# Kernel tuning notes

Measured on AMD Instinct MI355X. Metric: run time of the kernel, lower is better.

Reference implementation:

```python
import jax, jax.numpy as jnp
import numpy as np

# ---- Cl(3,0) algebra tables (basis: 1, e1, e2, e3, e12, e13, e23, e123) ----
def _build_algebra():
    dim = 8
    blades = sorted(range(dim), key=lambda b: (bin(b).count('1'), b))
    idx = {b: i for i, b in enumerate(blades)}
    C = np.zeros((dim, dim, dim), np.float32)
    for a in range(dim):
        for b in range(dim):
            s = 0; ash = a >> 1
            while ash:
                s += bin(ash & b).count('1'); ash >>= 1
            C[idx[a], idx[b], idx[a ^ b]] = -1.0 if (s & 1) else 1.0
    grades = np.array([bin(b).count('1') for b in blades])
    rev = np.array([(-1.0) ** (g * (g - 1) // 2) for g in grades], np.float32)
    gmask = np.zeros((4, dim), np.float32)
    gmask[grades, np.arange(dim)] = 1.0
    return C, rev, gmask, grades

_C_np, _REV_np, _GM_np, _GRADES = _build_algebra()
CAYLEY = jnp.asarray(_C_np)          # [8,8,8] sparse multiplication table
REV = jnp.asarray(_REV_np)           # reverse signs per blade
GMASK = jnp.asarray(_GM_np)          # [4,8] grade selector
BV_IDX = jnp.asarray(np.where(_GRADES == 2)[0])  # bivector slots [4,5,6]
G1_IDX = jnp.asarray(np.where(_GRADES == 1)[0])  # vector slots [1,2,3]

EPS = 1e-6
H_NUM, DEPTH, A_NUM, DISC, TEMP = 8, 3, 5, 0.99, 1.0

def gp(a, b):
    return jnp.einsum('...i,...j,ijk->...k', a, b, CAYLEY)

def reverse(x):
    return x * REV

def grade_energy(x):  # [...,8] -> [...,4] per-grade sum of squares
    return jnp.einsum('...d,gd->...g', x * x, GMASK)

def scatter_bv(c):  # [...,3] bivector coeffs -> full multivector [...,8]
    out = jnp.zeros(c.shape[:-1] + (8,), c.dtype)
    return out.at[..., BV_IDX].set(c)

def mv_exp_biv(b):  # exp of pure bivector in Cl(3,0): cos|B| + sinc|B| * B
    t = jnp.sqrt(jnp.sum(b * b, -1))
    small = t < 1e-6
    ts = jnp.where(small, 1.0, t)
    sinc = jnp.where(small, 1.0 - t * t / 6.0, jnp.sin(ts) / ts)
    return (sinc[..., None] * b).at[..., 0].add(jnp.cos(t))

def clayernorm(x, w):  # normalize by mean multivector norm across channels
    n = jnp.sqrt(jnp.sum(x * x, -1) + EPS)          # [...,C]
    denom = jnp.mean(n, -1, keepdims=True)[..., None] + EPS
    return x * w[:, None] / denom

def ggelu(x):  # gate multivector by GELU of its norm
    n = jnp.sqrt(jnp.sum(x * x, -1, keepdims=True) + EPS)
    return x * jax.nn.gelu(n) / (n + EPS)

def clinear(x, W, b):  # channel-mixing per blade: [O,C]x[...,C,8]
    return jnp.einsum('oc,...cd->...od', W, x) + b

def rotor_apply(x, bv):  # per-channel rotor sandwich, bv [C,3]
    R = mv_exp_biv(-0.5 * scatter_bv(bv))  # [C,8]
    return gp(gp(R, x), reverse(R))

def predict(x, nw, lw, lb, vw, vb, pw, pb):
    h = clayernorm(x, nw)
    h = clinear(h, lw, lb)
    h = ggelu(h)
    value = h[..., 0] @ vw + vb                      # grade-0 -> [N,1]
    g1 = h[..., G1_IDX].reshape(h.shape[0], -1)       # grade-1 flat
    policy = g1 @ pw + pb                             # [N,A]
    return policy, value

def dynamics(x, action, act_bv, nw, rbv, lw, lb, rw, rb):
    bv = act_bv[action]                               # [N,3]
    R = mv_exp_biv(-0.5 * scatter_bv(bv))[:, None, :]  # [N,1,8]
    ns = gp(gp(R, x), reverse(R))                     # rotor sandwich
    h = clayernorm(ns, nw)
    h = ggelu(h)
    h = rotor_apply(h, rbv)
    h = clinear(h, lw, lb)
    ns = ns + h                                       # residual GA block
    reward = ns[..., 0] @ rw + rb
    return reward, ns


def setup_inputs() -> dict:
    key = jax.random.key(0)
    ks = jax.random.split(key, 16)
    B, C, mid = 512, 256, 128
    f = jnp.float32
    return {
        'state': jax.random.normal(ks[0], (B, C, 8), f),
        'hyp_bv': jax.random.normal(ks[1], (H_NUM, 3), f) * 0.05,
        'sp_w1': jax.random.normal(ks[2], (4, 32), f) * 0.3,
        'sp_b1': jnp.zeros((32,), f),
        'sp_w2': jax.random.normal(ks[3], (32, 1), f) * 0.3,
        'sp_b2': jnp.zeros((1,), f),
        'p_norm_w': jnp.ones((C,), f),
        'p_lin_w': jax.random.normal(ks[4], (mid, C), f) / np.sqrt(C),
        'p_lin_b': jnp.zeros((mid, 8), f),
        'p_vw': jax.random.normal(ks[5], (mid, 1), f) * 0.1,
        'p_vb': jnp.zeros((1,), f),
        'p_pw': jax.random.normal(ks[6], (mid * 3, A_NUM), f) * 0.1,
        'p_pb': jnp.zeros((A_NUM,), f),
        'act_bv': jax.random.normal(ks[7], (A_NUM, 3), f) * 0.1,
        'd_norm_w': jnp.ones((C,), f),
        'd_rotor_bv': jax.random.normal(ks[8], (C, 3), f) * 0.05,
        'd_lin_w': jax.random.normal(ks[9], (C, C), f) / np.sqrt(C),
        'd_lin_b': jnp.zeros((C, 8), f),
        'd_rw': jax.random.normal(ks[10], (C, 1), f) * 0.1,
        'd_rb': jnp.zeros((1,), f),
    }


def reference(state, hyp_bv, sp_w1, sp_b1, sp_w2, sp_b2,
              p_norm_w, p_lin_w, p_lin_b, p_vw, p_vb, p_pw, p_pb,
              act_bv, d_norm_w, d_rotor_bv, d_lin_w, d_lin_b, d_rw, d_rb):
    B, C, D = state.shape
    H, A = H_NUM, A_NUM
    # hypothesis generation: H independent rotors applied to state
    R = mv_exp_biv(-0.5 * scatter_bv(hyp_bv))          # [H,8]
    hyp = gp(gp(R[None, :, None, :], state[:, None, :, :]),
             reverse(R)[None, :, None, :])             # [B,H,C,8]
    # exploration parameter from grade-norm features
    norms = jnp.sqrt(grade_energy(state) + 1e-12)       # [B,C,4]
    pooled = norms.mean(1)                              # [B,4]
    theta = jnp.maximum(pooled @ sp_w1 + sp_b1, 0.0) @ sp_w2 + sp_b2
    explore = jnp.abs(jnp.tanh(theta))                  # [B,1]
    N = B * H
    hf = hyp.reshape(N, C, D)
    exp_bh = jnp.broadcast_to(explore[:, None, :], (B, H, 1)).reshape(N, 1)
    noise = jax.random.normal(jax.random.key(42), (DEPTH, N, A), state.dtype) * 0.3
    hyp_values = jnp.zeros((B, H), state.dtype)
    first_actions = jnp.zeros((N,), jnp.int32)
    for d in range(DEPTH):  # fixed small depth loop; H vectorized
        policy, value = predict(hf, p_norm_w, p_lin_w, p_lin_b, p_vw, p_vb, p_pw, p_pb)
        bv_e = grade_energy(hf)[:, :, 2].mean(1, keepdims=True)  # bivector energy
        scores = policy + exp_bh * bv_e * noise[d]
        action = jnp.argmax(scores, -1)
        if d == 0:
            first_actions = action
        reward, hf = dynamics(hf, action, act_bv, d_norm_w, d_rotor_bv,
                              d_lin_w, d_lin_b, d_rw, d_rb)
        hyp_values = hyp_values + (DISC ** d) * reward.reshape(B, H)
    _, tv = predict(hf, p_norm_w, p_lin_w, p_lin_b, p_vw, p_vb, p_pw, p_pb)
    hyp_values = hyp_values + (DISC ** DEPTH) * tv.reshape(B, H)
    weights = jax.nn.softmax(hyp_values / TEMP, -1)     # [B,H]
    oh = jax.nn.one_hot(first_actions.reshape(B, H), A, dtype=state.dtype)
    ap = jnp.sum(weights[..., None] * oh, 1)            # [B,A]
    return ap / jnp.clip(jnp.sum(ap, -1, keepdims=True), 1e-8)
```

## Files before the change

### kernel.cpp

```cpp
#include <hip/hip_runtime.h>
#include <math.h>


#define NOISE_MODE 0
#define DEV static __device__ __forceinline__

constexpr int Bz = 512;
constexpr int Cz = 256;
constexpr int MIDz = 128;
constexpr int Hz = 8;
constexpr int Nz = 4096;
constexpr int Az = 5;
constexpr int NOISE_PER_D = Nz * Az;

constexpr size_t OFF_ROTH  = 0;
constexpr size_t OFF_ROTA  = OFF_ROTH + 64;
constexpr size_t OFF_ROTC  = OFF_ROTA + 40;
constexpr size_t OFF_EXPL  = OFF_ROTC + 2048;
constexpr size_t OFF_HV    = OFF_EXPL + 512;
constexpr size_t OFF_FIRST = OFF_HV + 4096;
constexpr size_t OFF_WTP   = OFF_FIRST + 4096;
constexpr size_t OFF_WTD   = OFF_WTP + (size_t)Cz * MIDz;
constexpr size_t OFF_A     = OFF_WTD + (size_t)Cz * Cz;

DEV void gp8(const float* a, const float* b, float* c) {
  c[0] = a[0]*b[0]+a[1]*b[1]+a[2]*b[2]+a[3]*b[3]-a[4]*b[4]-a[5]*b[5]-a[6]*b[6]-a[7]*b[7];
  c[1] = a[0]*b[1]+a[1]*b[0]-a[2]*b[4]-a[3]*b[5]+a[4]*b[2]+a[5]*b[3]-a[6]*b[7]-a[7]*b[6];
  c[2] = a[0]*b[2]+a[2]*b[0]+a[1]*b[4]-a[4]*b[1]-a[3]*b[6]+a[6]*b[3]+a[5]*b[7]+a[7]*b[5];
  c[3] = a[0]*b[3]+a[3]*b[0]+a[1]*b[5]-a[5]*b[1]+a[2]*b[6]-a[6]*b[2]-a[4]*b[7]-a[7]*b[4];
  c[4] = a[0]*b[4]+a[4]*b[0]+a[1]*b[2]-a[2]*b[1]-a[5]*b[6]+a[6]*b[5]+a[3]*b[7]+a[7]*b[3];
  c[5] = a[0]*b[5]+a[5]*b[0]+a[1]*b[3]-a[3]*b[1]+a[4]*b[6]-a[6]*b[4]-a[2]*b[7]-a[7]*b[2];
  c[6] = a[0]*b[6]+a[6]*b[0]+a[2]*b[3]-a[3]*b[2]-a[4]*b[5]+a[5]*b[4]+a[1]*b[7]+a[7]*b[1];
  c[7] = a[0]*b[7]+a[7]*b[0]+a[1]*b[6]+a[6]*b[1]+a[3]*b[4]+a[4]*b[3]-a[2]*b[5]-a[5]*b[2];
}

DEV void sandwich8(const float* R, const float* x, float* y) {
  float t[8];
  gp8(R, x, t);
  float Rr[8] = {R[0], R[1], R[2], R[3], -R[4], -R[5], -R[6], -R[7]};
  gp8(t, Rr, y);
}

DEV void rotor_from_bv(const float* bv, float* R) {
  float c4 = -0.5f * bv[0], c5 = -0.5f * bv[1], c6 = -0.5f * bv[2];
  float t = sqrtf(c4*c4 + c5*c5 + c6*c6);
  float sinc = (t < 1e-6f) ? (1.0f - t*t/6.0f) : (sinf(t)/t);
  R[0] = cosf(t); R[1] = 0.f; R[2] = 0.f; R[3] = 0.f;
  R[4] = sinc*c4; R[5] = sinc*c5; R[6] = sinc*c6; R[7] = 0.f;
}

DEV unsigned tf_rotl(unsigned v, int n) { return (v << n) | (v >> (32 - n)); }

DEV void threefry2x32(unsigned x0, unsigned x1, unsigned& o0, unsigned& o1) {
  const unsigned k0 = 0u, k1 = 42u;
  const unsigned k2 = k0 ^ k1 ^ 0x1BD11BDAu;
  x0 += k0; x1 += k1;
#define TF_R(r) { x0 += x1; x1 = tf_rotl(x1, r); x1 ^= x0; }
  TF_R(13) TF_R(15) TF_R(26) TF_R(6)
  x0 += k1; x1 += k2 + 1u;
  TF_R(17) TF_R(29) TF_R(16) TF_R(24)
  x0 += k2; x1 += k0 + 2u;
  TF_R(13) TF_R(15) TF_R(26) TF_R(6)
  x0 += k0; x1 += k1 + 3u;
  TF_R(17) TF_R(29) TF_R(16) TF_R(24)
  x0 += k1; x1 += k2 + 4u;
  TF_R(13) TF_R(15) TF_R(26) TF_R(6)
  x0 += k2; x1 += k0 + 5u;
#undef TF_R
  o0 = x0; o1 = x1;
}

DEV float erfinv32(float x) {
  float w = -log1pf(-x * x);
  float p;
  if (w < 5.0f) {
    w = w - 2.5f;
    p = 2.81022636e-08f;
    p = fmaf(p, w, 3.43273939e-07f);
    p = fmaf(p, w, -3.5233877e-06f);
    p = fmaf(p, w, -4.39150654e-06f);
    p = fmaf(p, w, 0.00021858087f);
    p = fmaf(p, w, -0.00125372503f);
    p = fmaf(p, w, -0.00417768164f);
    p = fmaf(p, w, 0.246640727f);
    p = fmaf(p, w, 1.50140941f);
  } else {
    w = sqrtf(w) - 3.0f;
    p = -0.000200214257f;
    p = fmaf(p, w, 0.000100950558f);
    p = fmaf(p, w, 0.00134934322f);
    p = fmaf(p, w, -0.00367342844f);
    p = fmaf(p, w, 0.00573950773f);
    p = fmaf(p, w, -0.0076224613f);
    p = fmaf(p, w, 0.00943887047f);
    p = fmaf(p, w, 1.00167406f);
    p = fmaf(p, w, 2.83297682f);
  }
  return p * x;
}

DEV float noise_val(int d, int r, int a) {
  unsigned idx = (unsigned)(d * NOISE_PER_D + r * Az + a);
  unsigned o0, o1, bits;
#if NOISE_MODE == 0
  threefry2x32(0u, idx, o0, o1);
  bits = o0 ^ o1;
#elif NOISE_MODE == 1
  const unsigned HALF = (unsigned)(3 * NOISE_PER_D) / 2u;
  unsigned j = (idx < HALF) ? idx : idx - HALF;
  threefry2x32(j, j + HALF, o0, o1);
  bits = (idx < HALF) ? o0 : o1;
#elif NOISE_MODE == 2
  threefry2x32(0u, idx, o0, o1);
  bits = o1;
#else
  threefry2x32(0u, idx, o0, o1);
  bits = o0;
#endif
  const float MINV = __uint_as_float(0xBF7FFFFFu);
  float f = __uint_as_float((bits >> 9) | 0x3F800000u) - 1.0f;
  float u = fmaxf(MINV, f * 2.0f + MINV);
  const float SQRT2 = __uint_as_float(0x3FB504F3u);
  return (SQRT2 * erfinv32(u)) * 0.3f;
}

DEV float gelu_tanh(float x) {
  float x3 = (x * x) * x;
  float t = tanhf(0.7978845608028654f * (x + 0.044715f * x3));
  return x * (0.5f * (1.0f + t));
}

DEV void pred_gemm(const float4* __restrict__ X, int l, float invd,
                   const float* __restrict__ WtP, const float* __restrict__ plb,
                   float hh[2][8]) {
  float pacc[2][8] = {{0,0,0,0,0,0,0,0},{0,0,0,0,0,0,0,0}};
  const float2* Wp2 = (const float2*)WtP;
#pragma unroll 4
  for (int c = 0; c < Cz; c++) {
    float4 xa = X[c], xb = X[Cz + c];
    float xv[8] = {xa.x, xa.y, xa.z, xa.w, xb.x, xb.y, xb.z, xb.w};
    float2 wv = Wp2[(size_t)c * 64 + l];
#pragma unroll
    for (int dd = 0; dd < 8; dd++) {
      pacc[0][dd] = fmaf(wv.x, xv[dd], pacc[0][dd]);
      pacc[1][dd] = fmaf(wv.y, xv[dd], pacc[1][dd]);
    }
  }
#pragma unroll
  for (int j = 0; j < 2; j++) {
    int o = 2 * l + j;
    float nsq = 0.f;
#pragma unroll
    for (int dd = 0; dd < 8; dd++) {
      hh[j][dd] = fmaf(pacc[j][dd], invd, plb[o * 8 + dd]);
      nsq += hh[j][dd] * hh[j][dd];
    }
    float nn = sqrtf(nsq + 1e-6f);
    float sc = gelu_tanh(nn) / (nn + 1e-6f);
#pragma unroll
    for (int dd = 0; dd < 8; dd++) hh[j][dd] *= sc;
  }
}


__global__ void k_prep(const float* __restrict__ hyp_bv, const float* __restrict__ act_bv,
                       const float* __restrict__ rot_bv, const float* __restrict__ plw,
                       const float* __restrict__ pnw, const float* __restrict__ dlw,
                       float* __restrict__ rotH, float* __restrict__ rotA,
                       float* __restrict__ rotC, float* __restrict__ hyp_val,
                       float* __restrict__ WtP, float* __restrict__ WtD) {
  int t = blockIdx.x * 256 + threadIdx.x;
  if (t < Cz * Cz)   { int c = t >> 8, o = t & 255; WtD[t] = dlw[o * Cz + c]; }
  if (t < Cz * MIDz) { int c = t >> 7, o = t & 127; WtP[t] = plw[o * Cz + c] * pnw[c]; }
  if (t < Nz) hyp_val[t] = 0.f;
  if (t < 8) rotor_from_bv(hyp_bv + t * 3, rotH + t * 8);
  else if (t < 13) rotor_from_bv(act_bv + (t - 8) * 3, rotA + (t - 8) * 8);
  else if (t >= 16 && t < 16 + Cz) rotor_from_bv(rot_bv + (t - 16) * 3, rotC + (t - 16) * 8);
}

__global__ void k_explore(const float* __restrict__ state, const float* __restrict__ w1,
                          const float* __restrict__ b1, const float* __restrict__ w2,
                          const float* __restrict__ b2, float* __restrict__ explore) {
  int b = blockIdx.x, c = threadIdx.x;
  const float4* xp = (const float4*)(state + ((size_t)b * Cz + c) * 8);
  float4 lo = xp[0], hi = xp[1];
  float g0 = lo.x * lo.x;
  float g1 = lo.y * lo.y + lo.z * lo.z + lo.w * lo.w;
  float g2 = hi.x * hi.x + hi.y * hi.y + hi.z * hi.z;
  float g3 = hi.w * hi.w;
  __shared__ float4 sm[256];
  sm[c] = make_float4(sqrtf(g0 + 1e-12f), sqrtf(g1 + 1e-12f),
                      sqrtf(g2 + 1e-12f), sqrtf(g3 + 1e-12f));
  __syncthreads();
  for (int s = 128; s > 0; s >>= 1) {
    if (c < s) {
      sm[c].x += sm[c + s].x; sm[c].y += sm[c + s].y;
      sm[c].z += sm[c + s].z; sm[c].w += sm[c + s].w;
    }
    __syncthreads();
  }
  if (c == 0) {
    float pooled[4] = {sm[0].x / 256.f, sm[0].y / 256.f, sm[0].z / 256.f, sm[0].w / 256.f};
    float theta = b2[0];
    for (int j = 0; j < 32; j++) {
      float hj = b1[j];
      for (int g = 0; g < 4; g++) hj = fmaf(pooled[g], w1[g * 32 + j], hj);
      hj = fmaxf(hj, 0.f);
      theta = fmaf(hj, w2[j], theta);
    }
    explore[b] = fabsf(tanhf(theta));
  }
}

__global__ __launch_bounds__(256, 4) void k_step(
    const float* __restrict__ src, float* __restrict__ dst, int apply_hyp,
    int dstep, int do_term,
    const float* __restrict__ rotH, const float* __restrict__ rotA,
    const float* __restrict__ rotC, const float* __restrict__ WtP,
    const float* __restrict__ plb, const float* __restrict__ pw,
    const float* __restrict__ pb, const float* __restrict__ vw,
    const float* __restrict__ vb, const float* __restrict__ dnw,
    const float* __restrict__ WtD, const float* __restrict__ dlb,
    const float* __restrict__ rw, const float* __restrict__ rb,
    const float* __restrict__ explore, float* __restrict__ hyp_val,
    int* __restrict__ first_act, float discf, float termdisc) {
  __shared__ float4 xs[4][2 * Cz];
  int w = threadIdx.x >> 6, l = threadIdx.x & 63;
  int r = blockIdx.x * 4 + w;
  int b = r >> 3, h = r & 7;
  float4* X = xs[w];
  const float* row = apply_hyp ? (src + (size_t)b * Cz * 8) : (src + (size_t)r * Cz * 8);
  float Rh[8];
  if (apply_hyp) {
#pragma unroll
    for (int i = 0; i < 8; i++) Rh[i] = rotH[h * 8 + i];
  }
  float nsum = 0.f, bsum = 0.f;
#pragma unroll
  for (int k = 0; k < 4; k++) {
    int c = 4 * l + k;
    const float4* xp = (const float4*)(row + (size_t)c * 8);
    float4 v0 = xp[0], v1 = xp[1];
    float x[8] = {v0.x, v0.y, v0.z, v0.w, v1.x, v1.y, v1.z, v1.w};
    if (apply_hyp) {
      float t[8];
      sandwich8(Rh, x, t);
#pragma unroll
      for (int i = 0; i < 8; i++) x[i] = t[i];
    }
    float ss = 0.f;
#pragma unroll
    for (int i = 0; i < 8; i++) ss += x[i] * x[i];
    nsum += sqrtf(ss + 1e-6f);
    bsum += x[4] * x[4] + x[5] * x[5] + x[6] * x[6];
    X[c]      = make_float4(x[0], x[1], x[2], x[3]);
    X[Cz + c] = make_float4(x[4], x[5], x[6], x[7]);
  }
#pragma unroll
  for (int m = 1; m < 64; m <<= 1) {
    nsum += __shfl_xor(nsum, m);
    bsum += __shfl_xor(bsum, m);
  }
  float invd = 1.0f / (nsum / 256.f + 1e-6f);
  float bv_e = bsum / 256.f;
  __syncthreads();

  float hh[2][8];
  pred_gemm(X, l, invd, WtP, plb, hh);
  float pol[Az] = {0, 0, 0, 0, 0};
#pragma unroll
  for (int j = 0; j < 2; j++) {
    int o = 2 * l + j;
#pragma unroll
    for (int k = 0; k < 3; k++) {
      float v = hh[j][1 + k];
      const float* pwj = pw + (size_t)(o * 3 + k) * Az;
#pragma unroll
      for (int a = 0; a < Az; a++) pol[a] = fmaf(v, pwj[a], pol[a]);
    }
  }
#pragma unroll
  for (int m = 1; m < 64; m <<= 1) {
#pragma unroll
    for (int a = 0; a < Az; a++) pol[a] += __shfl_xor(pol[a], m);
  }
  float coef = explore[b] * bv_e;
  float sa = -INFINITY;
  if (l < Az) sa = (pol[l] + pb[l]) + coef * noise_val(dstep, r, l);
  int best = 0;
  float bs = -INFINITY;
#pragma unroll
  for (int a = 0; a < Az; a++) {
    float s = __shfl(sa, a);
    if (s > bs) { bs = s; best = a; }
  }
  if (dstep == 0 && l == 0) first_act[r] = best;

  float Ra[8];
#pragma unroll
  for (int i = 0; i < 8; i++) Ra[i] = rotA[best * 8 + i];
  float y[4][8];
  float nsum2 = 0.f;
#pragma unroll
  for (int k = 0; k < 4; k++) {
    int c = 4 * l + k;
    float4 xa = X[c], xb = X[Cz + c];
    float x[8] = {xa.x, xa.y, xa.z, xa.w, xb.x, xb.y, xb.z, xb.w};
    sandwich8(Ra, x, y[k]);
    float ss = 0.f;
#pragma unroll
    for (int i = 0; i < 8; i++) ss += y[k][i] * y[k][i];
    nsum2 += sqrtf(ss + 1e-6f);
  }
#pragma unroll
  for (int m = 1; m < 64; m <<= 1) nsum2 += __shfl_xor(nsum2, m);
  float invd2 = 1.0f / (nsum2 / 256.f + 1e-6f);

#pragma unroll
  for (int k = 0; k < 4; k++) {
    int c = 4 * l + k;
    float sc = dnw[c] * invd2;
    float hch[8];
    float nsq = 0.f;
#pragma unroll
    for (int i = 0; i < 8; i++) { hch[i] = y[k][i] * sc; nsq += hch[i] * hch[i]; }
    float nn = sqrtf(nsq + 1e-6f);
    float ge = gelu_tanh(nn) / (nn + 1e-6f);
#pragma unroll
    for (int i = 0; i < 8; i++) hch[i] *= ge;
    float Rc[8];
    const float4* rp = (const float4*)(rotC + (size_t)c * 8);
    float4 r0 = rp[0], r1 = rp[1];
    Rc[0] = r0.x; Rc[1] = r0.y; Rc[2] = r0.z; Rc[3] = r0.w;
    Rc[4] = r1.x; Rc[5] = r1.y; Rc[6] = r1.z; Rc[7] = r1.w;
    float hp[8];
    sandwich8(Rc, hch, hp);
    X[c]      = make_float4(hp[0], hp[1], hp[2], hp[3]);
    X[Cz + c] = make_float4(hp[4], hp[5], hp[6], hp[7]);
  }
  __syncthreads();

  float acc[4][8];
#pragma unroll
  for (int g = 0; g < 4; g++) {
    int o = 4 * l + g;
#pragma unroll
    for (int dd = 0; dd < 8; dd++) acc[g][dd] = y[g][dd] + dlb[o * 8 + dd];
  }
  const float4* Wd4 = (const float4*)WtD;
#pragma unroll 4
  for (int c = 0; c < Cz; c++) {
    float4 xa = X[c], xb = X[Cz + c];
    float xv[8] = {xa.x, xa.y, xa.z, xa.w, xb.x, xb.y, xb.z, xb.w};
    float4 w4 = Wd4[(size_t)c * 64 + l];
#pragma unroll
    for (int dd = 0; dd < 8; dd++) {
      acc[0][dd] = fmaf(w4.x, xv[dd], acc[0][dd]);
      acc[1][dd] = fmaf(w4.y, xv[dd], acc[1][dd]);
      acc[2][dd] = fmaf(w4.z, xv[dd], acc[2][dd]);
      acc[3][dd] = fmaf(w4.w, xv[dd], acc[3][dd]);
    }
  }

  float rsum = 0.f;
  float hv_add;
  if (!do_term) {
    float* drow = dst + (size_t)r * Cz * 8;
#pragma unroll
    for (int g = 0; g < 4; g++) {
      int o = 4 * l + g;
      rsum = fmaf(acc[g][0], rw[o], rsum);
      float4* op = (float4*)(drow + (size_t)o * 8);
      op[0] = make_float4(acc[g][0], acc[g][1], acc[g][2], acc[g][3]);
      op[1] = make_float4(acc[g][4], acc[g][5], acc[g][6], acc[g][7]);
    }
#pragma unroll
    for (int m = 1; m < 64; m <<= 1) rsum += __shfl_xor(rsum, m);
    hv_add = discf * (rsum + rb[0]);
  } else {
    __syncthreads();
    float tsum = 0.f;
#pragma unroll
    for (int g = 0; g < 4; g++) {
      int o = 4 * l + g;
      rsum = fmaf(acc[g][0], rw[o], rsum);
      float ss = 0.f;
#pragma unroll
      for (int dd = 0; dd < 8; dd++) ss += acc[g][dd] * acc[g][dd];
      tsum += sqrtf(ss + 1e-6f);
      X[o]      = make_float4(acc[g][0], acc[g][1], acc[g][2], acc[g][3]);
      X[Cz + o] = make_float4(acc[g][4], acc[g][5], acc[g][6], acc[g][7]);
    }
#pragma unroll
    for (int m = 1; m < 64; m <<= 1) {
      rsum += __shfl_xor(rsum, m);
      tsum += __shfl_xor(tsum, m);
    }
    float invd3 = 1.0f / (tsum / 256.f + 1e-6f);
    __syncthreads();
    float th[2][8];
    pred_gemm(X, l, invd3, WtP, plb, th);
    float v = fmaf(th[0][0], vw[2 * l], th[1][0] * vw[2 * l + 1]);
#pragma unroll
    for (int m = 1; m < 64; m <<= 1) v += __shfl_xor(v, m);
    hv_add = discf * (rsum + rb[0]) + termdisc * (v + vb[0]);
  }
  if (l == 0) hyp_val[r] += hv_add;
}

__global__ void k_out(const float* __restrict__ hyp_val, const int* __restrict__ first_act,
                      float* __restrict__ out) {
  int b = blockIdx.x * blockDim.x + threadIdx.x;
  if (b >= Bz) return;
  float hv[Hz];
  float m = -INFINITY;
#pragma unroll
  for (int h = 0; h < Hz; h++) { hv[h] = hyp_val[b * Hz + h]; m = fmaxf(m, hv[h]); }
  float e[Hz];
  float se = 0.f;
#pragma unroll
  for (int h = 0; h < Hz; h++) { e[h] = expf(hv[h] - m); se += e[h]; }
  float ap[Az] = {0, 0, 0, 0, 0};
#pragma unroll
  for (int h = 0; h < Hz; h++) ap[first_act[b * Hz + h]] += e[h] / se;
  float tot = 0.f;
#pragma unroll
  for (int a = 0; a < Az; a++) tot += ap[a];
  float dn = fmaxf(tot, 1e-8f);
#pragma unroll
  for (int a = 0; a < Az; a++) out[b * Az + a] = ap[a] / dn;
}


extern "C" void kernel_launch(void* const* d_in, const int* in_sizes, int n_in,
                              void* d_out, int out_size, void* d_ws, size_t ws_size,
                              hipStream_t stream) {
  const float* state      = (const float*)d_in[0];
  const float* hyp_bv     = (const float*)d_in[1];
  const float* sp_w1      = (const float*)d_in[2];
  const float* sp_b1      = (const float*)d_in[3];
  const float* sp_w2      = (const float*)d_in[4];
  const float* sp_b2      = (const float*)d_in[5];
  const float* p_norm_w   = (const float*)d_in[6];
  const float* p_lin_w    = (const float*)d_in[7];
  const float* p_lin_b    = (const float*)d_in[8];
  const float* p_vw       = (const float*)d_in[9];
  const float* p_vb       = (const float*)d_in[10];
  const float* p_pw       = (const float*)d_in[11];
  const float* p_pb       = (const float*)d_in[12];
  const float* act_bv     = (const float*)d_in[13];
  const float* d_norm_w   = (const float*)d_in[14];
  const float* d_rotor_bv = (const float*)d_in[15];
  const float* d_lin_w    = (const float*)d_in[16];
  const float* d_lin_b    = (const float*)d_in[17];
  const float* d_rw       = (const float*)d_in[18];
  const float* d_rb       = (const float*)d_in[19];
  float* out = (float*)d_out;
  float* ws  = (float*)d_ws;

  float* rotH    = ws + OFF_ROTH;
  float* rotA    = ws + OFF_ROTA;
  float* rotC    = ws + OFF_ROTC;
  float* explore = ws + OFF_EXPL;
  float* hyp_val = ws + OFF_HV;
  int*   first   = (int*)(ws + OFF_FIRST);
  float* WtP     = ws + OFF_WTP;
  float* WtD     = ws + OFF_WTD;
  float* bufA    = ws + OFF_A;

  k_prep<<<256, 256, 0, stream>>>(hyp_bv, act_bv, d_rotor_bv, p_lin_w, p_norm_w,
                                  d_lin_w, rotH, rotA, rotC, hyp_val, WtP, WtD);
  k_explore<<<Bz, 256, 0, stream>>>(state, sp_w1, sp_b1, sp_w2, sp_b2, explore);

  const float d1 = 0.99f, d2 = 0.99f * 0.99f, d3 = 0.99f * 0.99f * 0.99f;
  k_step<<<Nz / 4, 256, 0, stream>>>(state, bufA, 1, 0, 0, rotH, rotA, rotC, WtP,
                                     p_lin_b, p_pw, p_pb, p_vw, p_vb, d_norm_w, WtD,
                                     d_lin_b, d_rw, d_rb, explore, hyp_val, first,
                                     1.0f, 0.f);
  k_step<<<Nz / 4, 256, 0, stream>>>(bufA, bufA, 0, 1, 0, rotH, rotA, rotC, WtP,
                                     p_lin_b, p_pw, p_pb, p_vw, p_vb, d_norm_w, WtD,
                                     d_lin_b, d_rw, d_rb, explore, hyp_val, first,
                                     d1, 0.f);
  k_step<<<Nz / 4, 256, 0, stream>>>(bufA, bufA, 0, 2, 1, rotH, rotA, rotC, WtP,
                                     p_lin_b, p_pw, p_pb, p_vw, p_vb, d_norm_w, WtD,
                                     d_lin_b, d_rw, d_rb, explore, hyp_val, first,
                                     d2, d3);
  k_out<<<2, 256, 0, stream>>>(hyp_val, first, out);
}
```

Before: 379.1 us.

## Use packed FP32 FMA and swizzle shared-memory channel layout in GEMMs

```diff
diff --git a/kernel.cpp b/kernel.cpp
--- a/kernel.cpp
+++ b/kernel.cpp
@@ -4,6 +4,9 @@
 
 #define NOISE_MODE 0
 #define DEV static __device__ __forceinline__
+
+typedef float v2f __attribute__((ext_vector_type(2)));
+DEV v2f fma2(v2f a, v2f b, v2f c) { return __builtin_elementwise_fma(a, b, c); }
 
 constexpr int Bz = 512;
 constexpr int Cz = 256;
@@ -130,20 +133,32 @@
   return x * (0.5f * (1.0f + t));
 }
 
+DEV int SL(int c) { return ((c & 3) << 6) + (c >> 2); }
+
 DEV void pred_gemm(const float4* __restrict__ X, int l, float invd,
                    const float* __restrict__ WtP, const float* __restrict__ plb,
                    float hh[2][8]) {
-  float pacc[2][8] = {{0,0,0,0,0,0,0,0},{0,0,0,0,0,0,0,0}};
+  v2f pacc[2][4] = {{{0,0},{0,0},{0,0},{0,0}},{{0,0},{0,0},{0,0},{0,0}}};
   const float2* Wp2 = (const float2*)WtP;
-#pragma unroll 4
-  for (int c = 0; c < Cz; c++) {
-    float4 xa = X[c], xb = X[Cz + c];
-    float xv[8] = {xa.x, xa.y, xa.z, xa.w, xb.x, xb.y, xb.z, xb.w};
-    float2 wv = Wp2[(size_t)c * 64 + l];
-#pragma unroll
-    for (int dd = 0; dd < 8; dd++) {
-      pacc[0][dd] = fmaf(wv.x, xv[dd], pacc[0][dd]);
-      pacc[1][dd] = fmaf(wv.y, xv[dd], pacc[1][dd]);
+#pragma unroll 2
+  for (int c4 = 0; c4 < 64; c4++) {
+#pragma unroll
+    for (int k = 0; k < 4; k++) {
+      int c = 4 * c4 + k;
+      float4 xa = X[(k << 6) + c4];
+      float4 xb = X[Cz + (k << 6) + c4];
+      float2 wv = Wp2[(size_t)c * 64 + l];
+      v2f w0 = {wv.x, wv.x}, w1 = {wv.y, wv.y};
+      v2f x0 = {xa.x, xa.y}, x1 = {xa.z, xa.w};
+      v2f x2 = {xb.x, xb.y}, x3 = {xb.z, xb.w};
+      pacc[0][0] = fma2(w0, x0, pacc[0][0]);
+      pacc[0][1] = fma2(w0, x1, pacc[0][1]);
+      pacc[0][2] = fma2(w0, x2, pacc[0][2]);
+      pacc[0][3] = fma2(w0, x3, pacc[0][3]);
+      pacc[1][0] = fma2(w1, x0, pacc[1][0]);
+      pacc[1][1] = fma2(w1, x1, pacc[1][1]);
+      pacc[1][2] = fma2(w1, x2, pacc[1][2]);
+      pacc[1][3] = fma2(w1, x3, pacc[1][3]);
     }
   }
 #pragma unroll
@@ -152,7 +167,8 @@
     float nsq = 0.f;
 #pragma unroll
     for (int dd = 0; dd < 8; dd++) {
-      hh[j][dd] = fmaf(pacc[j][dd], invd, plb[o * 8 + dd]);
+      float av = (dd & 1) ? pacc[j][dd >> 1].y : pacc[j][dd >> 1].x;
+      hh[j][dd] = fmaf(av, invd, plb[o * 8 + dd]);
       nsq += hh[j][dd] * hh[j][dd];
     }
     float nn = sqrtf(nsq + 1e-6f);
@@ -253,8 +269,9 @@
     for (int i = 0; i < 8; i++) ss += x[i] * x[i];
     nsum += sqrtf(ss + 1e-6f);
     bsum += x[4] * x[4] + x[5] * x[5] + x[6] * x[6];
-    X[c]      = make_float4(x[0], x[1], x[2], x[3]);
-    X[Cz + c] = make_float4(x[4], x[5], x[6], x[7]);
+    int sl = (k << 6) + l;
+    X[sl]      = make_float4(x[0], x[1], x[2], x[3]);
+    X[Cz + sl] = make_float4(x[4], x[5], x[6], x[7]);
   }
 #pragma unroll
   for (int m = 1; m < 64; m <<= 1) {
@@ -303,8 +320,8 @@
   float nsum2 = 0.f;
 #pragma unroll
   for (int k = 0; k < 4; k++) {
-    int c = 4 * l + k;
-    float4 xa = X[c], xb = X[Cz + c];
+    int sl = (k << 6) + l;
+    float4 xa = X[sl], xb = X[Cz + sl];
     float x[8] = {xa.x, xa.y, xa.z, xa.w, xb.x, xb.y, xb.z, xb.w};
     sandwich8(Ra, x, y[k]);
     float ss = 0.f;
@@ -335,30 +352,50 @@
     Rc[4] = r1.x; Rc[5] = r1.y; Rc[6] = r1.z; Rc[7] = r1.w;
     float hp[8];
     sandwich8(Rc, hch, hp);
-    X[c]      = make_float4(hp[0], hp[1], hp[2], hp[3]);
-    X[Cz + c] = make_float4(hp[4], hp[5], hp[6], hp[7]);
+    int sl = (k << 6) + l;
+    X[sl]      = make_float4(hp[0], hp[1], hp[2], hp[3]);
+    X[Cz + sl] = make_float4(hp[4], hp[5], hp[6], hp[7]);
   }
   __syncthreads();
 
-  float acc[4][8];
+  v2f acc[4][4];
 #pragma unroll
   for (int g = 0; g < 4; g++) {
     int o = 4 * l + g;
 #pragma unroll
-    for (int dd = 0; dd < 8; dd++) acc[g][dd] = y[g][dd] + dlb[o * 8 + dd];
+    for (int p = 0; p < 4; p++) {
+      acc[g][p].x = y[g][2 * p]     + dlb[o * 8 + 2 * p];
+      acc[g][p].y = y[g][2 * p + 1] + dlb[o * 8 + 2 * p + 1];
+    }
   }
   const float4* Wd4 = (const float4*)WtD;
-#pragma unroll 4
-  for (int c = 0; c < Cz; c++) {
-    float4 xa = X[c], xb = X[Cz + c];
-    float xv[8] = {xa.x, xa.y, xa.z, xa.w, xb.x, xb.y, xb.z, xb.w};
-    float4 w4 = Wd4[(size_t)c * 64 + l];
-#pragma unroll
-    for (int dd = 0; dd < 8; dd++) {
-      acc[0][dd] = fmaf(w4.x, xv[dd], acc[0][dd]);
-      acc[1][dd] = fmaf(w4.y, xv[dd], acc[1][dd]);
-      acc[2][dd] = fmaf(w4.z, xv[dd], acc[2][dd]);
-      acc[3][dd] = fmaf(w4.w, xv[dd], acc[3][dd]);
+#pragma unroll 2
+  for (int c4 = 0; c4 < 64; c4++) {
+#pragma unroll
+    for (int k = 0; k < 4; k++) {
+      int c = 4 * c4 + k;
+      float4 xa = X[(k << 6) + c4];
+      float4 xb = X[Cz + (k << 6) + c4];
+      v2f x0 = {xa.x, xa.y}, x1 = {xa.z, xa.w};
+      v2f x2 = {xb.x, xb.y}, x3 = {xb.z, xb.w};
+      float4 w4 = Wd4[(size_t)c * 64 + l];
+      v2f w0 = {w4.x, w4.x}, w1 = {w4.y, w4.y}, w2 = {w4.z, w4.z}, w3 = {w4.w, w4.w};
+      acc[0][0] = fma2(w0, x0, acc[0][0]);
+      acc[0][1] = fma2(w0, x1, acc[0][1]);
+      acc[0][2] = fma2(w0, x2, acc[0][2]);
+      acc[0][3] = fma2(w0, x3, acc[0][3]);
+      acc[1][0] = fma2(w1, x0, acc[1][0]);
+      acc[1][1] = fma2(w1, x1, acc[1][1]);
+      acc[1][2] = fma2(w1, x2, acc[1][2]);
+      acc[1][3] = fma2(w1, x3, acc[1][3]);
+      acc[2][0] = fma2(w2, x0, acc[2][0]);
+      acc[2][1] = fma2(w2, x1, acc[2][1]);
+      acc[2][2] = fma2(w2, x2, acc[2][2]);
+      acc[2][3] = fma2(w2, x3, acc[2][3]);
+      acc[3][0] = fma2(w3, x0, acc[3][0]);
+      acc[3][1] = fma2(w3, x1, acc[3][1]);
+      acc[3][2] = fma2(w3, x2, acc[3][2]);
+      acc[3][3] = fma2(w3, x3, acc[3][3]);
     }
   }
 
@@ -369,10 +406,10 @@
 #pragma unroll
     for (int g = 0; g < 4; g++) {
       int o = 4 * l + g;
-      rsum = fmaf(acc[g][0], rw[o], rsum);
+      rsum = fmaf(acc[g][0].x, rw[o], rsum);
       float4* op = (float4*)(drow + (size_t)o * 8);
-      op[0] = make_float4(acc[g][0], acc[g][1], acc[g][2], acc[g][3]);
-      op[1] = make_float4(acc[g][4], acc[g][5], acc[g][6], acc[g][7]);
+      op[0] = make_float4(acc[g][0].x, acc[g][0].y, acc[g][1].x, acc[g][1].y);
+      op[1] = make_float4(acc[g][2].x, acc[g][2].y, acc[g][3].x, acc[g][3].y);
     }
 #pragma unroll
     for (int m = 1; m < 64; m <<= 1) rsum += __shfl_xor(rsum, m);
@@ -383,13 +420,14 @@
 #pragma unroll
     for (int g = 0; g < 4; g++) {
       int o = 4 * l + g;
-      rsum = fmaf(acc[g][0], rw[o], rsum);
+      rsum = fmaf(acc[g][0].x, rw[o], rsum);
       float ss = 0.f;
 #pragma unroll
-      for (int dd = 0; dd < 8; dd++) ss += acc[g][dd] * acc[g][dd];
+      for (int p = 0; p < 4; p++) ss += acc[g][p].x * acc[g][p].x + acc[g][p].y * acc[g][p].y;
       tsum += sqrtf(ss + 1e-6f);
-      X[o]      = make_float4(acc[g][0], acc[g][1], acc[g][2], acc[g][3]);
-      X[Cz + o] = make_float4(acc[g][4], acc[g][5], acc[g][6], acc[g][7]);
+      int sl = (g << 6) + l;
+      X[sl]      = make_float4(acc[g][0].x, acc[g][0].y, acc[g][1].x, acc[g][1].y);
+      X[Cz + sl] = make_float4(acc[g][2].x, acc[g][2].y, acc[g][3].x, acc[g][3].y);
     }
 #pragma unroll
     for (int m = 1; m < 64; m <<= 1) {
```

After: 434.5 us. +14.6%, slower.

## Split each row across two waves to halve per-thread GEMM outputs

Applied to the files above, without the earlier changes.

```diff
diff --git a/kernel.cpp b/kernel.cpp
--- a/kernel.cpp
+++ b/kernel.cpp
@@ -130,36 +130,37 @@
   return x * (0.5f * (1.0f + t));
 }
 
-DEV void pred_gemm(const float4* __restrict__ X, int l, float invd,
-                   const float* __restrict__ WtP, const float* __restrict__ plb,
-                   float hh[2][8]) {
-  float pacc[2][8] = {{0,0,0,0,0,0,0,0},{0,0,0,0,0,0,0,0}};
-  const float2* Wp2 = (const float2*)WtP;
-#pragma unroll 4
-  for (int c = 0; c < Cz; c++) {
-    float4 xa = X[c], xb = X[Cz + c];
-    float xv[8] = {xa.x, xa.y, xa.z, xa.w, xb.x, xb.y, xb.z, xb.w};
-    float2 wv = Wp2[(size_t)c * 64 + l];
-#pragma unroll
-    for (int dd = 0; dd < 8; dd++) {
-      pacc[0][dd] = fmaf(wv.x, xv[dd], pacc[0][dd]);
-      pacc[1][dd] = fmaf(wv.y, xv[dd], pacc[1][dd]);
-    }
-  }
-#pragma unroll
-  for (int j = 0; j < 2; j++) {
-    int o = 2 * l + j;
-    float nsq = 0.f;
-#pragma unroll
-    for (int dd = 0; dd < 8; dd++) {
-      hh[j][dd] = fmaf(pacc[j][dd], invd, plb[o * 8 + dd]);
-      nsq += hh[j][dd] * hh[j][dd];
-    }
-    float nn = sqrtf(nsq + 1e-6f);
-    float sc = gelu_tanh(nn) / (nn + 1e-6f);
-#pragma unroll
-    for (int dd = 0; dd < 8; dd++) hh[j][dd] *= sc;
-  }
+DEV void pred_gemm1(const float4* __restrict__ X, int o, float invd,
+                    const float* __restrict__ WtP, const float* __restrict__ plb,
+                    float hh[8]) {
+  float acc[8] = {0, 0, 0, 0, 0, 0, 0, 0};
+#pragma unroll 2
+  for (int c4 = 0; c4 < 64; c4++) {
+#pragma unroll
+    for (int k = 0; k < 4; k++) {
+      float4 xa = X[(k << 6) + c4];
+      float4 xb = X[Cz + (k << 6) + c4];
+      float wv = WtP[(size_t)(4 * c4 + k) * MIDz + o];
+      acc[0] = fmaf(wv, xa.x, acc[0]);
+      acc[1] = fmaf(wv, xa.y, acc[1]);
+      acc[2] = fmaf(wv, xa.z, acc[2]);
+      acc[3] = fmaf(wv, xa.w, acc[3]);
+      acc[4] = fmaf(wv, xb.x, acc[4]);
+      acc[5] = fmaf(wv, xb.y, acc[5]);
+      acc[6] = fmaf(wv, xb.z, acc[6]);
+      acc[7] = fmaf(wv, xb.w, acc[7]);
+    }
+  }
+  float nsq = 0.f;
+#pragma unroll
+  for (int dd = 0; dd < 8; dd++) {
+    hh[dd] = fmaf(acc[dd], invd, plb[o * 8 + dd]);
+    nsq += hh[dd] * hh[dd];
+  }
+  float nn = sqrtf(nsq + 1e-6f);
+  float sc = gelu_tanh(nn) / (nn + 1e-6f);
+#pragma unroll
+  for (int dd = 0; dd < 8; dd++) hh[dd] *= sc;
 }
 
 
@@ -212,7 +213,7 @@
   }
 }
 
-__global__ __launch_bounds__(256, 4) void k_step(
+__global__ __launch_bounds__(512, 8) void k_step(
     const float* __restrict__ src, float* __restrict__ dst, int apply_hyp,
     int dstep, int do_term,
     const float* __restrict__ rotH, const float* __restrict__ rotA,
@@ -225,10 +226,17 @@
     const float* __restrict__ explore, float* __restrict__ hyp_val,
     int* __restrict__ first_act, float discf, float termdisc) {
   __shared__ float4 xs[4][2 * Cz];
-  int w = threadIdx.x >> 6, l = threadIdx.x & 63;
-  int r = blockIdx.x * 4 + w;
+  __shared__ float rnorm[4][2][2];
+  __shared__ float rpol[4][2][Az];
+  __shared__ float rdy[4][2];
+  __shared__ float rrw[4][2];
+  __shared__ float rts[4][2];
+  __shared__ float rv[4][2];
+  int wave = threadIdx.x >> 6, l = threadIdx.x & 63;
+  int wr = wave >> 1, ww = wave & 1;
+  int r = blockIdx.x * 4 + wr;
   int b = r >> 3, h = r & 7;
-  float4* X = xs[w];
+  float4* X = xs[wr];
   const float* row = apply_hyp ? (src + (size_t)b * Cz * 8) : (src + (size_t)r * Cz * 8);
   float Rh[8];
   if (apply_hyp) {
@@ -237,7 +245,8 @@
   }
   float nsum = 0.f, bsum = 0.f;
 #pragma unroll
-  for (int k = 0; k < 4; k++) {
+  for (int k2 = 0; k2 < 2; k2++) {
+    int k = 2 * ww + k2;
     int c = 4 * l + k;
     const float4* xp = (const float4*)(row + (size_t)c * 8);
     float4 v0 = xp[0], v1 = xp[1];
@@ -253,40 +262,47 @@
     for (int i = 0; i < 8; i++) ss += x[i] * x[i];
     nsum += sqrtf(ss + 1e-6f);
     bsum += x[4] * x[4] + x[5] * x[5] + x[6] * x[6];
-    X[c]      = make_float4(x[0], x[1], x[2], x[3]);
-    X[Cz + c] = make_float4(x[4], x[5], x[6], x[7]);
+    int sl = (k << 6) + l;
+    X[sl]      = make_float4(x[0], x[1], x[2], x[3]);
+    X[Cz + sl] = make_float4(x[4], x[5], x[6], x[7]);
   }
 #pragma unroll
   for (int m = 1; m < 64; m <<= 1) {
     nsum += __shfl_xor(nsum, m);
     bsum += __shfl_xor(bsum, m);
   }
-  float invd = 1.0f / (nsum / 256.f + 1e-6f);
-  float bv_e = bsum / 256.f;
+  if (l == 0) { rnorm[wr][ww][0] = nsum; rnorm[wr][ww][1] = bsum; }
   __syncthreads();
 
-  float hh[2][8];
-  pred_gemm(X, l, invd, WtP, plb, hh);
+  float nT = rnorm[wr][0][0] + rnorm[wr][1][0];
+  float bT = rnorm[wr][0][1] + rnorm[wr][1][1];
+  float invd = 1.0f / (nT / 256.f + 1e-6f);
+  float bv_e = bT / 256.f;
+  int o1 = 64 * ww + l;
+  float hh[8];
+  pred_gemm1(X, o1, invd, WtP, plb, hh);
   float pol[Az] = {0, 0, 0, 0, 0};
 #pragma unroll
-  for (int j = 0; j < 2; j++) {
-    int o = 2 * l + j;
-#pragma unroll
-    for (int k = 0; k < 3; k++) {
-      float v = hh[j][1 + k];
-      const float* pwj = pw + (size_t)(o * 3 + k) * Az;
-#pragma unroll
-      for (int a = 0; a < Az; a++) pol[a] = fmaf(v, pwj[a], pol[a]);
-    }
+  for (int k = 0; k < 3; k++) {
+    float v = hh[1 + k];
+    const float* pwj = pw + (size_t)(o1 * 3 + k) * Az;
+#pragma unroll
+    for (int a = 0; a < Az; a++) pol[a] = fmaf(v, pwj[a], pol[a]);
   }
 #pragma unroll
   for (int m = 1; m < 64; m <<= 1) {
 #pragma unroll
     for (int a = 0; a < Az; a++) pol[a] += __shfl_xor(pol[a], m);
   }
+  if (l < Az) rpol[wr][ww][l] = pol[l];
+  __syncthreads();
+
   float coef = explore[b] * bv_e;
   float sa = -INFINITY;
-  if (l < Az) sa = (pol[l] + pb[l]) + coef * noise_val(dstep, r, l);
+  if (l < Az) {
+    float pfull = rpol[wr][0][l] + rpol[wr][1][l] + pb[l];
+    sa = pfull + coef * noise_val(dstep, r, l);
+  }
   int best = 0;
   float bs = -INFINITY;
 #pragma unroll
@@ -294,36 +310,40 @@
     float s = __shfl(sa, a);
     if (s > bs) { bs = s; best = a; }
   }
-  if (dstep == 0 && l == 0) first_act[r] = best;
+  if (dstep == 0 && ww == 0 && l == 0) first_act[r] = best;
 
   float Ra[8];
 #pragma unroll
   for (int i = 0; i < 8; i++) Ra[i] = rotA[best * 8 + i];
-  float y[4][8];
+  float y[2][8];
   float nsum2 = 0.f;
 #pragma unroll
-  for (int k = 0; k < 4; k++) {
-    int c = 4 * l + k;
-    float4 xa = X[c], xb = X[Cz + c];
+  for (int k2 = 0; k2 < 2; k2++) {
+    int k = 2 * ww + k2;
+    int sl = (k << 6) + l;
+    float4 xa = X[sl], xb = X[Cz + sl];
     float x[8] = {xa.x, xa.y, xa.z, xa.w, xb.x, xb.y, xb.z, xb.w};
-    sandwich8(Ra, x, y[k]);
+    sandwich8(Ra, x, y[k2]);
     float ss = 0.f;
 #pragma unroll
-    for (int i = 0; i < 8; i++) ss += y[k][i] * y[k][i];
+    for (int i = 0; i < 8; i++) ss += y[k2][i] * y[k2][i];
     nsum2 += sqrtf(ss + 1e-6f);
   }
 #pragma unroll
   for (int m = 1; m < 64; m <<= 1) nsum2 += __shfl_xor(nsum2, m);
-  float invd2 = 1.0f / (nsum2 / 256.f + 1e-6f);
-
-#pragma unroll
-  for (int k = 0; k < 4; k++) {
+  if (l == 0) rdy[wr][ww] = nsum2;
+  __syncthreads();
+
+  float invd2 = 1.0f / ((rdy[wr][0] + rdy[wr][1]) / 256.f + 1e-6f);
+#pragma unroll
+  for (int k2 = 0; k2 < 2; k2++) {
+    int k = 2 * ww + k2;
     int c = 4 * l + k;
     float sc = dnw[c] * invd2;
     float hch[8];
     float nsq = 0.f;
 #pragma unroll
-    for (int i = 0; i < 8; i++) { hch[i] = y[k][i] * sc; nsq += hch[i] * hch[i]; }
+    for (int i = 0; i < 8; i++) { hch[i] = y[k2][i] * sc; nsq += hch[i] * hch[i]; }
     float nn = sqrtf(nsq + 1e-6f);
     float ge = gelu_tanh(nn) / (nn + 1e-6f);
 #pragma unroll
@@ -335,77 +355,90 @@
     Rc[4] = r1.x; Rc[5] = r1.y; Rc[6] = r1.z; Rc[7] = r1.w;
     float hp[8];
     sandwich8(Rc, hch, hp);
-    X[c]      = make_float4(hp[0], hp[1], hp[2], hp[3]);
-    X[Cz + c] = make_float4(hp[4], hp[5], hp[6], hp[7]);
+    int sl = (k << 6) + l;
+    X[sl]      = make_float4(hp[0], hp[1], hp[2], hp[3]);
+    X[Cz + sl] = make_float4(hp[4], hp[5], hp[6], hp[7]);
   }
   __syncthreads();
 
-  float acc[4][8];
-#pragma unroll
-  for (int g = 0; g < 4; g++) {
-    int o = 4 * l + g;
-#pragma unroll
-    for (int dd = 0; dd < 8; dd++) acc[g][dd] = y[g][dd] + dlb[o * 8 + dd];
-  }
-  const float4* Wd4 = (const float4*)WtD;
-#pragma unroll 4
-  for (int c = 0; c < Cz; c++) {
-    float4 xa = X[c], xb = X[Cz + c];
-    float xv[8] = {xa.x, xa.y, xa.z, xa.w, xb.x, xb.y, xb.z, xb.w};
-    float4 w4 = Wd4[(size_t)c * 64 + l];
-#pragma unroll
-    for (int dd = 0; dd < 8; dd++) {
-      acc[0][dd] = fmaf(w4.x, xv[dd], acc[0][dd]);
-      acc[1][dd] = fmaf(w4.y, xv[dd], acc[1][dd]);
-      acc[2][dd] = fmaf(w4.z, xv[dd], acc[2][dd]);
-      acc[3][dd] = fmaf(w4.w, xv[dd], acc[3][dd]);
-    }
-  }
-
-  float rsum = 0.f;
-  float hv_add;
+  float acc[2][8];
+  int ob = 4 * l + 2 * ww;
+#pragma unroll
+  for (int k2 = 0; k2 < 2; k2++) {
+#pragma unroll
+    for (int dd = 0; dd < 8; dd++) acc[k2][dd] = y[k2][dd] + dlb[(ob + k2) * 8 + dd];
+  }
+#pragma unroll 2
+  for (int c4 = 0; c4 < 64; c4++) {
+#pragma unroll
+    for (int k = 0; k < 4; k++) {
+      float4 xa = X[(k << 6) + c4];
+      float4 xb = X[Cz + (k << 6) + c4];
+      float2 w2 = *(const float2*)&WtD[(size_t)(4 * c4 + k) * Cz + ob];
+      acc[0][0] = fmaf(w2.x, xa.x, acc[0][0]);
+      acc[0][1] = fmaf(w2.x, xa.y, acc[0][1]);
+      acc[0][2] = fmaf(w2.x, xa.z, acc[0][2]);
+      acc[0][3] = fmaf(w2.x, xa.w, acc[0][3]);
+      acc[0][4] = fmaf(w2.x, xb.x, acc[0][4]);
+      acc[0][5] = fmaf(w2.x, xb.y, acc[0][5]);
+      acc[0][6] = fmaf(w2.x, xb.z, acc[0][6]);
+      acc[0][7] = fmaf(w2.x, xb.w, acc[0][7]);
+      acc[1][0] = fmaf(w2.y, xa.x, acc[1][0]);
+      acc[1][1] = fmaf(w2.y, xa.y, acc[1][1]);
+      acc[1][2] = fmaf(w2.y, xa.z, acc[1][2]);
+      acc[1][3] = fmaf(w2.y, xa.w, acc[1][3]);
+      acc[1][4] = fmaf(w2.y, xb.x, acc[1][4]);
+      acc[1][5] = fmaf(w2.y, xb.y, acc[1][5]);
+      acc[1][6] = fmaf(w2.y, xb.z, acc[1][6]);
+      acc[1][7] = fmaf(w2.y, xb.w, acc[1][7]);
+    }
+  }
+
+  float rsum = fmaf(acc[0][0], rw[ob], acc[1][0] * rw[ob + 1]);
+#pragma unroll
+  for (int m = 1; m < 64; m <<= 1) rsum += __shfl_xor(rsum, m);
+  if (l == 0) rrw[wr][ww] = rsum;
+
   if (!do_term) {
     float* drow = dst + (size_t)r * Cz * 8;
 #pragma unroll
-    for (int g = 0; g < 4; g++) {
-      int o = 4 * l + g;
-      rsum = fmaf(acc[g][0], rw[o], rsum);
-      float4* op = (float4*)(drow + (size_t)o * 8);
-      op[0] = make_float4(acc[g][0], acc[g][1], acc[g][2], acc[g][3]);
-      op[1] = make_float4(acc[g][4], acc[g][5], acc[g][6], acc[g][7]);
-    }
-#pragma unroll
-    for (int m = 1; m < 64; m <<= 1) rsum += __shfl_xor(rsum, m);
-    hv_add = discf * (rsum + rb[0]);
+    for (int k2 = 0; k2 < 2; k2++) {
+      float4* op = (float4*)(drow + (size_t)(ob + k2) * 8);
+      op[0] = make_float4(acc[k2][0], acc[k2][1], acc[k2][2], acc[k2][3]);
+      op[1] = make_float4(acc[k2][4], acc[k2][5], acc[k2][6], acc[k2][7]);
+    }
+    __syncthreads();
+    if (ww == 0 && l == 0)
+      hyp_val[r] += discf * (rrw[wr][0] + rrw[wr][1] + rb[0]);
   } else {
     __syncthreads();
     float tsum = 0.f;
 #pragma unroll
-    for (int g = 0; g < 4; g++) {
-      int o = 4 * l + g;
-      rsum = fmaf(acc[g][0], rw[o], rsum);
+    for (int k2 = 0; k2 < 2; k2++) {
       float ss = 0.f;
 #pragma unroll
-      for (int dd = 0; dd < 8; dd++) ss += acc[g][dd] * acc[g][dd];
+      for (int dd = 0; dd < 8; dd++) ss += acc[k2][dd] * acc[k2][dd];
       tsum += sqrtf(ss + 1e-6f);
-      X[o]      = make_float4(acc[g][0], acc[g][1], acc[g][2], acc[g][3]);
-      X[Cz + o] = make_float4(acc[g][4], acc[g][5], acc[g][6], acc[g][7]);
-    }
-#pragma unroll
-    for (int m = 1; m < 64; m <<= 1) {
-      rsum += __shfl_xor(rsum, m);
-      tsum += __shfl_xor(tsum, m);
-    }
-    float invd3 = 1.0f / (tsum / 256.f + 1e-6f);
+      int sl = ((2 * ww + k2) << 6) + l;
+      X[sl]      = make_float4(acc[k2][0], acc[k2][1], acc[k2][2], acc[k2][3]);
+      X[Cz + sl] = make_float4(acc[k2][4], acc[k2][5], acc[k2][6], acc[k2][7]);
+    }
+#pragma unroll
+    for (int m = 1; m < 64; m <<= 1) tsum += __shfl_xor(tsum, m);
+    if (l == 0) rts[wr][ww] = tsum;
     __syncthreads();
-    float th[2][8];
-    pred_gemm(X, l, invd3, WtP, plb, th);
-    float v = fmaf(th[0][0], vw[2 * l], th[1][0] * vw[2 * l + 1]);
+    float invd3 = 1.0f / ((rts[wr][0] + rts[wr][1]) / 256.f + 1e-6f);
+    float th[8];
+    pred_gemm1(X, o1, invd3, WtP, plb, th);
+    float v = th[0] * vw[o1];
 #pragma unroll
     for (int m = 1; m < 64; m <<= 1) v += __shfl_xor(v, m);
-    hv_add = discf * (rsum + rb[0]) + termdisc * (v + vb[0]);
-  }
-  if (l == 0) hyp_val[r] += hv_add;
+    if (l == 0) rv[wr][ww] = v;
+    __syncthreads();
+    if (ww == 0 && l == 0)
+      hyp_val[r] += discf * (rrw[wr][0] + rrw[wr][1] + rb[0])
+                  + termdisc * (rv[wr][0] + rv[wr][1] + vb[0]);
+  }
 }
 
 __global__ void k_out(const float* __restrict__ hyp_val, const int* __restrict__ first_act,
@@ -473,15 +506,15 @@
   k_explore<<<Bz, 256, 0, stream>>>(state, sp_w1, sp_b1, sp_w2, sp_b2, explore);
 
   const float d1 = 0.99f, d2 = 0.99f * 0.99f, d3 = 0.99f * 0.99f * 0.99f;
-  k_step<<<Nz / 4, 256, 0, stream>>>(state, bufA, 1, 0, 0, rotH, rotA, rotC, WtP,
+  k_step<<<Nz / 4, 512, 0, stream>>>(state, bufA, 1, 0, 0, rotH, rotA, rotC, WtP,
                                      p_lin_b, p_pw, p_pb, p_vw, p_vb, d_norm_w, WtD,
                                      d_lin_b, d_rw, d_rb, explore, hyp_val, first,
                                      1.0f, 0.f);
-  k_step<<<Nz / 4, 256, 0, stream>>>(bufA, bufA, 0, 1, 0, rotH, rotA, rotC, WtP,
+  k_step<<<Nz / 4, 512, 0, stream>>>(bufA, bufA, 0, 1, 0, rotH, rotA, rotC, WtP,
                                      p_lin_b, p_pw, p_pb, p_vw, p_vb, d_norm_w, WtD,
                                      d_lin_b, d_rw, d_rb, explore, hyp_val, first,
                                      d1, 0.f);
-  k_step<<<Nz / 4, 256, 0, stream>>>(bufA, bufA, 0, 2, 1, rotH, rotA, rotC, WtP,
+  k_step<<<Nz / 4, 512, 0, stream>>>(bufA, bufA, 0, 2, 1, rotH, rotA, rotC, WtP,
                                      p_lin_b, p_pw, p_pb, p_vw, p_vb, d_norm_w, WtD,
                                      d_lin_b, d_rw, d_rb, explore, hyp_val, first,
                                      d2, d3);
```

Result: slower. 495.9 us (+30.8%).
